# Kernel tuning notes

Measured on AMD Instinct MI355X. Metric: run time of the kernel, lower is better.

The kernel has to match this reference:

```python
import jax, jax.numpy as jnp
import numpy as np

SHOTS = 5  # kernel height of all convs; K must equal SHOTS


def _conv2d(x, w, b, stride, pad):
    # x: (N, C, H, W), w: (O, I, kh, kw)
    y = jax.lax.conv_general_dilated(
        x, w, window_strides=stride, padding=pad,
        dimension_numbers=("NCHW", "OIHW", "NCHW"))
    return y + b[None, :, None, None]


def setup_inputs() -> dict:
    key = jax.random.key(0)
    ks = jax.random.split(key, 10)
    B, N, K, D, NQ = 8, 20, SHOTS, 230, 200
    s = 0.05
    return {
        "S": jax.random.normal(ks[0], (B, N, K, D), jnp.float32),
        "Q": jax.random.normal(ks[1], (B, NQ, D), jnp.float32),
        "fc_w": jax.random.normal(ks[2], (D, D), jnp.float32) * s,
        "fc_b": jax.random.normal(ks[3], (D,), jnp.float32) * s,
        "conv1_w": jax.random.normal(ks[4], (32, 1, SHOTS, 1), jnp.float32) * s,
        "conv1_b": jax.random.normal(ks[5], (32,), jnp.float32) * s,
        "conv2_w": jax.random.normal(ks[6], (64, 32, SHOTS, 1), jnp.float32) * s,
        "conv2_b": jax.random.normal(ks[7], (64,), jnp.float32) * s,
        "convf_w": jax.random.normal(ks[8], (1, 64, SHOTS, 1), jnp.float32) * s,
        "convf_b": jax.random.normal(ks[9], (1,), jnp.float32) * s,
    }


def reference(S, Q, fc_w, fc_b, conv1_w, conv1_b, conv2_w, conv2_b, convf_w, convf_b):
    B, N, K, D = S.shape
    NQ = Q.shape[1]
    p = SHOTS // 2

    # ---- conv score extraction over the K (shot) axis ----
    x = S.reshape(B * N, 1, K, D)
    x = jax.nn.relu(_conv2d(x, conv1_w, conv1_b, (1, 1), [(p, p), (0, 0)]))
    x = jax.nn.relu(_conv2d(x, conv2_w, conv2_b, (1, 1), [(p, p), (0, 0)]))
    # dropout is identity in eval mode
    x = jax.nn.relu(_conv2d(x, convf_w, convf_b, (SHOTS, 1), [(0, 0), (0, 0)]))
    score = x.reshape(B, N, D)  # BxNxD

    # ---- hybrid attention prototype ----
    # fc applied to broadcast-expanded tensors == fc applied once, then broadcast
    Sf = S @ fc_w.T + fc_b            # B x N x K x D
    Qf = Q @ fc_w.T + fc_b            # B x NQ x D
    if K == 1:
        S_repre = jnp.broadcast_to(S.mean(-2)[:, None], (B, NQ, N, D))
    else:
        # tanh(S_fc * Q_fc).sum(-1) -> softmax over K
        t = jnp.tanh(Sf[:, None, :, :, :] * Qf[:, :, None, None, :])  # B,NQ,N,K,D
        att = jax.nn.softmax(t.sum(-1), axis=-1)                      # B,NQ,N,K
        S_repre = jnp.einsum("bqnk,bnkd->bqnd", att, S)               # B,NQ,N,D

    # ---- weighted squared L2 distance ----
    diff = S_repre - Q[:, :, None, :]                                  # B,NQ,N,D
    logits = -jnp.sum(diff * diff * score[:, None, :, :] * 700.0, axis=-1)  # B,NQ,N
    return (logits, S)
```

## Files before the change

### kernel.cpp

```cpp
#include <hip/hip_runtime.h>
#include <hip/hip_bf16.h>

typedef _Float16 f16x8 __attribute__((ext_vector_type(8)));
typedef float f32x4 __attribute__((ext_vector_type(4)));

#define BB 8
#define NN 20
#define KK 5
#define DD 230
#define NQ 200

#define NB_BFC 240
#define NB_BP  200
#define NB_CONV 575
#define NB_FC2 38
#define NB_ATT 800
#define NB_CP 90

__global__ void k_pre(const float* __restrict__ fc_w,
                      const float* __restrict__ w2, const float* __restrict__ b2,
                      const float* __restrict__ wf,
                      _Float16* __restrict__ Bfc, _Float16* __restrict__ Bp,
                      float2* __restrict__ tblg) {
    const int bid = blockIdx.x, tid = threadIdx.x;
    if (bid < NB_BFC) {
        int g = bid * 256 + tid;
        int kg = g & 31;
        int ncl = (g >> 5) & 15;
        int tk = g >> 9;
        int nt = tk >> 3, ks = tk & 7;
        int n = nt * 16 + ncl, k = ks * 32 + kg;
        float val = (n < DD && k < DD) ? fc_w[n * DD + k] : 0.f;
        Bfc[g] = (_Float16)val;
    } else {
        int g = (bid - NB_BFC) * 256 + tid;
        int kg = g & 31;
        int ncl = (g >> 5) & 15;
        int tk = g >> 9;
        int nt = tk / 5, ks = tk - nt * 5;
        int n = nt * 16 + ncl, k = ks * 32 + kg;
        int o = n / 5, i = n % 5;
        int c = k / 5, j = k - c * 5;
        int t = j - i + 2;
        float val = (t >= 0 && t < 5) ? w2[(o * 32 + c) * 5 + t] : 0.f;
        Bp[g] = (_Float16)val;
        if (g < 320) {
            int o2 = g / 5, i2 = g % 5;
            tblg[g] = make_float2(b2[o2], wf[o2 * 5 + i2]);
        }
    }
}

__global__ __launch_bounds__(512)
void k_main(const float* __restrict__ S, const float* __restrict__ Q,
            const float* __restrict__ w1, const float* __restrict__ b1,
            const _Float16* __restrict__ Bp, const _Float16* __restrict__ Bfc,
            const float2* __restrict__ tblg, float* __restrict__ sc,
            const float* __restrict__ fc_b,
            float* __restrict__ Sf, float* __restrict__ Qf) {
    __shared__ __align__(16) _Float16 XU[64 * 264];
    __shared__ float xfp[8][16];
    const int bid = blockIdx.x, tid = threadIdx.x;
    const int lane = tid & 63;
    const int w = __builtin_amdgcn_readfirstlane(tid >> 6);
    const int ncl = lane & 15;
    const int kg8 = (lane >> 4) * 8;
    const int g4 = lane >> 4;

    if (bid >= NB_CONV) {
        const int m0 = (bid - NB_CONV) * 64;
        for (int e = tid; e < 64 * 58; e += 512) {
            int row = e / 58, c4 = e - row * 58;
            int grow = m0 + row;
            float4 v = make_float4(0.f, 0.f, 0.f, 0.f);
            if (grow < 2400) {
                const float* inp = (grow < 800) ? S + (size_t)grow * DD
                                                : Q + (size_t)(grow - 800) * DD;
                if (c4 < 57) v = *(const float4*)&inp[c4 * 4];
                else { v.x = inp[228]; v.y = inp[229]; }
            }
            _Float16* xp = &XU[row * 264 + c4 * 4];
            xp[0] = (_Float16)v.x; xp[1] = (_Float16)v.y;
            xp[2] = (_Float16)v.z; xp[3] = (_Float16)v.w;
        }
        for (int e = tid; e < 64 * 16; e += 512) {
            int row = e >> 4, cc = 232 + (e & 15) * 2;
            *(unsigned int*)&XU[row * 264 + cc] = 0u;
        }
        __syncthreads();

        const int msub = w & 3;
        const int ngrp = w >> 2;
        f16x8 af[8];
#pragma unroll
        for (int ks = 0; ks < 8; ks++)
            af[ks] = *(const f16x8*)&XU[(msub * 16 + ncl) * 264 + ks * 32 + kg8];

        const int nt0 = ngrp * 8;
        const int ntn = ngrp ? 7 : 8;
        for (int ti = 0; ti < ntn; ti++) {
            const int nt = nt0 + ti;
            const _Float16* bp = Bfc + ((size_t)nt * 8 * 16) * 32;
            f32x4 a = {0.f, 0.f, 0.f, 0.f};
#pragma unroll
            for (int ks = 0; ks < 8; ks++) {
                f16x8 br = *(const f16x8*)&bp[(ks * 16 + ncl) * 32 + kg8];
                a = __builtin_amdgcn_mfma_f32_16x16x32_f16(af[ks], br, a, 0, 0, 0);
            }
            const int n = nt * 16 + ncl;
            const float bias = fc_b[n < DD ? n : DD - 1];
            if (n < DD) {
#pragma unroll
                for (int r = 0; r < 4; r++) {
                    int grow = m0 + msub * 16 + g4 * 4 + r;
                    if (grow < 800)
                        Sf[(size_t)grow * DD + n] = (a[r] + bias) * 2.8853900817779268f;
                    else if (grow < 2400)
                        Qf[(size_t)(grow - 800) * DD + n] = a[r] + bias;
                }
            }
        }
        return;
    }

    const int m0 = bid * 64;
    {
        const int m = m0 + lane;
        const int img = m / DD;
        const int d = m - img * DD;
        const float* sp = S + (size_t)img * KK * DD + d;
        float in5[5];
#pragma unroll
        for (int j = 0; j < 5; j++) in5[j] = sp[j * DD];
#pragma unroll
        for (int cc = 0; cc < 4; cc++) {
            int c = w * 4 + cc;
            float wl[5];
#pragma unroll
            for (int t = 0; t < 5; t++) wl[t] = w1[c * 5 + t];
            float bb = b1[c];
#pragma unroll
            for (int i = 0; i < 5; i++) {
                float a = bb;
#pragma unroll
                for (int t = 0; t < 5; t++) {
                    int j = i + t - 2;
                    if (j >= 0 && j < 5) a = fmaf(wl[t], in5[j], a);
                }
                XU[lane * 168 + c * 5 + i] = (_Float16)fmaxf(a, 0.f);
            }
        }
    }
    __syncthreads();

    const int msub = w & 3;
    const int gq = w >> 2;
    f16x8 af[5];
#pragma unroll
    for (int ks = 0; ks < 5; ks++)
        af[ks] = *(const f16x8*)&XU[(msub * 16 + ncl) * 168 + ks * 32 + kg8];

    float xf = 0.f;
    for (int t10 = 0; t10 < 10; t10++) {
        const int nt = gq * 10 + t10;
        const _Float16* bp = Bp + ((size_t)nt * 5 * 16) * 32;
        f32x4 a = {0.f, 0.f, 0.f, 0.f};
#pragma unroll
        for (int ks = 0; ks < 5; ks++) {
            f16x8 br = *(const f16x8*)&bp[(ks * 16 + ncl) * 32 + kg8];
            a = __builtin_amdgcn_mfma_f32_16x16x32_f16(br, af[ks], a, 0, 0, 0);
        }
        float2 tb[4];
#pragma unroll
        for (int r = 0; r < 4; r++) tb[r] = tblg[nt * 16 + g4 * 4 + r];
#pragma unroll
        for (int r = 0; r < 4; r++)
            xf = fmaf(fmaxf(a[r] + tb[r].x, 0.f), tb[r].y, xf);
    }
    xf += __shfl_xor(xf, 16, 64);
    xf += __shfl_xor(xf, 32, 64);
    if (lane < 16) xfp[w][lane] = xf;
    __syncthreads();
    if (tid < 64) {
        const int ms = tid >> 4, j = tid & 15;
        sc[m0 + ms * 16 + j] = xfp[ms][j] + xfp[ms + 4][j];
    }
}

__global__ __launch_bounds__(512)
void k_att(const float* __restrict__ Sf, const float* __restrict__ Qf,
           const float* __restrict__ S, const float* __restrict__ Q,
           const float* __restrict__ sc, const float* __restrict__ convf_b,
           float* __restrict__ out, float* __restrict__ Scopy) {
    __shared__ float Sft[25][232];
    __shared__ float Ls[8][25];
    const int bid = blockIdx.x, tid = threadIdx.x;
    if (bid >= NB_ATT) {
        int g = (bid - NB_ATT) * 512 + tid;
        if (g < 46000) ((float4*)Scopy)[g] = ((const float4*)S)[g];
        return;
    }
    const int lane = tid & 63, wv = tid >> 6;
    const int qg = bid % 25;
    const int nq = (bid / 25) & 3;
    const int b  = bid / 100;
    const int q  = qg * 8 + wv, n0 = nq * 5;
    const float LOG2E = 1.4426950408889634f;
    const float bf0 = convf_b[0];

    const float* sfb = Sf + ((size_t)b * 100 + n0 * 5) * DD;
    for (int e = tid; e < 25 * DD; e += 512) Sft[e / DD][e % DD] = sfb[e];
    __syncthreads();

    float qf[4];
    const float* qfp = Qf + ((size_t)b * NQ + q) * DD;
#pragma unroll
    for (int i = 0; i < 4; i++) {
        int d = lane + 64 * i;
        qf[i] = (d < DD) ? qfp[d] : 0.f;
    }
    for (int idx = 0; idx < 25; idx++) {
        float racc = 0.f;
#pragma unroll
        for (int i = 0; i < 4; i++) {
            int d = lane + 64 * i;
            float s = (d < DD) ? Sft[idx][d] : 0.f;
            float e = __builtin_amdgcn_exp2f(s * qf[i]);
            racc += __builtin_amdgcn_rcpf(e + 1.f);
        }
#pragma unroll
        for (int off = 32; off > 0; off >>= 1) racc += __shfl_xor(racc, off, 64);
        if (lane == 0) Ls[wv][idx] = fmaf(-2.f, racc, 256.f);
    }

    float qr[4];
    const float* qp = Q + ((size_t)b * NQ + q) * DD;
#pragma unroll
    for (int i = 0; i < 4; i++) {
        int d = lane + 64 * i;
        qr[i] = (d < DD) ? qp[d] : 0.f;
    }
    for (int nl = 0; nl < 5; nl++) {
        const float* lp = Ls[wv] + nl * 5;
        float v0 = lp[0], v1 = lp[1], v2 = lp[2], v3 = lp[3], v4 = lp[4];
        float m = fmaxf(fmaxf(fmaxf(v0, v1), fmaxf(v2, v3)), v4);
        float e0 = __builtin_amdgcn_exp2f((v0 - m) * LOG2E);
        float e1 = __builtin_amdgcn_exp2f((v1 - m) * LOG2E);
        float e2 = __builtin_amdgcn_exp2f((v2 - m) * LOG2E);
        float e3 = __builtin_amdgcn_exp2f((v3 - m) * LOG2E);
        float e4 = __builtin_amdgcn_exp2f((v4 - m) * LOG2E);
        float inv = __builtin_amdgcn_rcpf(e0 + e1 + e2 + e3 + e4);
        float a0 = e0 * inv, a1 = e1 * inv, a2 = e2 * inv, a3 = e3 * inv, a4 = e4 * inv;
        const int n = n0 + nl;
        const float* spn = S + (size_t)(b * NN + n) * KK * DD;
        const float* s0 = sc + (size_t)(b * NN + n) * DD;
        float acc = 0.f;
#pragma unroll
        for (int i = 0; i < 4; i++) {
            int d = lane + 64 * i;
            if (d < DD) {
                float rep = a0 * spn[d] + a1 * spn[DD + d] + a2 * spn[2 * DD + d]
                          + a3 * spn[3 * DD + d] + a4 * spn[4 * DD + d];
                float df = rep - qr[i];
                float scw = fmaxf(s0[d] + bf0, 0.f) * 700.f;
                acc = fmaf(df * df, scw, acc);
            }
        }
#pragma unroll
        for (int off = 32; off > 0; off >>= 1) acc += __shfl_xor(acc, off, 64);
        if (lane == 0) out[((size_t)b * NQ + q) * NN + n] = -acc;
    }
}

extern "C" void kernel_launch(void* const* d_in, const int* in_sizes, int n_in,
                              void* d_out, int out_size, void* d_ws, size_t ws_size,
                              hipStream_t stream) {
    const float* S       = (const float*)d_in[0];
    const float* Q       = (const float*)d_in[1];
    const float* fc_w    = (const float*)d_in[2];
    const float* fc_b    = (const float*)d_in[3];
    const float* conv1_w = (const float*)d_in[4];
    const float* conv1_b = (const float*)d_in[5];
    const float* conv2_w = (const float*)d_in[6];
    const float* conv2_b = (const float*)d_in[7];
    const float* convf_w = (const float*)d_in[8];
    const float* convf_b = (const float*)d_in[9];
    float* out = (float*)d_out;

    float* ws = (float*)d_ws;
    float* Sf  = ws;
    float* Qf  = Sf + 184000;
    float* sc  = Qf + 368000;
    _Float16* Bp  = (_Float16*)(sc + 36800);
    _Float16* Bfc = Bp + 51200;
    float2* tblg  = (float2*)(Bfc + 61440);

    k_pre<<<NB_BFC + NB_BP, 256, 0, stream>>>(
        fc_w, conv2_w, conv2_b, convf_w, Bfc, Bp, tblg);
    k_main<<<NB_CONV + NB_FC2, 512, 0, stream>>>(
        S, Q, conv1_w, conv1_b, Bp, Bfc, tblg, sc, fc_b, Sf, Qf);
    k_att<<<NB_ATT + NB_CP, 512, 0, stream>>>(
        Sf, Qf, S, Q, sc, convf_b, out, out + (size_t)BB * NQ * NN);
}
```

Measured before the change: 75.77 us.

## Restructure attention kernel to use MFMA row-sums over fp16 tanh tiles

The attention kernel now processes all 20 classes per block (200 blocks instead of 800). It stages all 100 Sf rows of a batch in shared memory as fp16, computes tanh values per element, and sums them with an MFMA against a ones vector instead of doing cross-lane shuffle reductions. Qf gets a padded row stride so it can be read with vector loads, and one loop in the conv kernel gets an unroll-2 pragma. The trade-offs are fp16 rounding of the tanh inputs and outputs, and fewer, larger blocks, which may lower occupancy.

```diff
diff --git a/kernel.cpp b/kernel.cpp
--- a/kernel.cpp
+++ b/kernel.cpp
@@ -9,13 +9,19 @@
 #define KK 5
 #define DD 230
 #define NQ 200
+#define QST 232
 
 #define NB_BFC 240
 #define NB_BP  200
 #define NB_CONV 575
 #define NB_FC2 38
-#define NB_ATT 800
+#define NB_ATT 200
 #define NB_CP 90
+
+static __device__ __forceinline__ unsigned int pk2(float a, float b) {
+    union { __fp16 h[2] __attribute__((aligned(4))); unsigned int u; } v;
+    v.h[0] = (__fp16)a; v.h[1] = (__fp16)b; return v.u;
+}
 
 __global__ void k_pre(const float* __restrict__ fc_w,
                       const float* __restrict__ w2, const float* __restrict__ b2,
@@ -116,7 +122,7 @@
                     if (grow < 800)
                         Sf[(size_t)grow * DD + n] = (a[r] + bias) * 2.8853900817779268f;
                     else if (grow < 2400)
-                        Qf[(size_t)(grow - 800) * DD + n] = a[r] + bias;
+                        Qf[(size_t)(grow - 800) * QST + n] = a[r] + bias;
                 }
             }
         }
@@ -161,6 +167,7 @@
         af[ks] = *(const f16x8*)&XU[(msub * 16 + ncl) * 168 + ks * 32 + kg8];
 
     float xf = 0.f;
+#pragma unroll 2
     for (int t10 = 0; t10 < 10; t10++) {
         const int nt = gq * 10 + t10;
         const _Float16* bp = Bp + ((size_t)nt * 5 * 16) * 32;
@@ -192,56 +199,79 @@
            const float* __restrict__ S, const float* __restrict__ Q,
            const float* __restrict__ sc, const float* __restrict__ convf_b,
            float* __restrict__ out, float* __restrict__ Scopy) {
-    __shared__ float Sft[25][232];
-    __shared__ float Ls[8][25];
+    __shared__ __align__(16) _Float16 SfT[112 * 264];
+    __shared__ __align__(16) float Lw[8][112];
     const int bid = blockIdx.x, tid = threadIdx.x;
     if (bid >= NB_ATT) {
         int g = (bid - NB_ATT) * 512 + tid;
         if (g < 46000) ((float4*)Scopy)[g] = ((const float4*)S)[g];
         return;
     }
-    const int lane = tid & 63, wv = tid >> 6;
-    const int qg = bid % 25;
-    const int nq = (bid / 25) & 3;
-    const int b  = bid / 100;
-    const int q  = qg * 8 + wv, n0 = nq * 5;
+    const int lane = tid & 63;
+    const int w = __builtin_amdgcn_readfirstlane(tid >> 6);
+    const int b = bid / 25, qg = bid % 25;
+    const int q = qg * 8 + w;
+    const int ncl = lane & 15;
+    const int g4 = lane >> 4;
+    const int kg8 = g4 * 8;
     const float LOG2E = 1.4426950408889634f;
     const float bf0 = convf_b[0];
 
-    const float* sfb = Sf + ((size_t)b * 100 + n0 * 5) * DD;
-    for (int e = tid; e < 25 * DD; e += 512) Sft[e / DD][e % DD] = sfb[e];
+    const float* sfb = Sf + (size_t)b * 100 * DD;
+    for (int e = tid; e < 112 * 132; e += 512) {
+        int row = e / 132, c2 = e - row * 132;
+        unsigned int u = 0u;
+        if (row < 100 && c2 <= 114) {
+            float2 v = *(const float2*)&sfb[row * DD + 2 * c2];
+            u = pk2(v.x, v.y);
+        }
+        *(unsigned int*)&SfT[row * 264 + 2 * c2] = u;
+    }
     __syncthreads();
 
-    float qf[4];
-    const float* qfp = Qf + ((size_t)b * NQ + q) * DD;
-#pragma unroll
-    for (int i = 0; i < 4; i++) {
-        int d = lane + 64 * i;
-        qf[i] = (d < DD) ? qfp[d] : 0.f;
-    }
-    for (int idx = 0; idx < 25; idx++) {
-        float racc = 0.f;
-#pragma unroll
-        for (int i = 0; i < 4; i++) {
-            int d = lane + 64 * i;
-            float s = (d < DD) ? Sft[idx][d] : 0.f;
-            float e = __builtin_amdgcn_exp2f(s * qf[i]);
-            racc += __builtin_amdgcn_rcpf(e + 1.f);
-        }
-#pragma unroll
-        for (int off = 32; off > 0; off >>= 1) racc += __shfl_xor(racc, off, 64);
-        if (lane == 0) Ls[wv][idx] = fmaf(-2.f, racc, 256.f);
+    f16x8 ones;
+#pragma unroll
+    for (int j = 0; j < 8; j++) ones[j] = (_Float16)1.f;
+    f32x4 acc[7];
+#pragma unroll
+    for (int t = 0; t < 7; t++) acc[t] = (f32x4){0.f, 0.f, 0.f, 0.f};
+
+    const float* qfp = Qf + (size_t)(b * NQ + q) * QST;
+    for (int ks = 0; ks < 8; ks++) {
+        f32x4 qa = *(const f32x4*)&qfp[ks * 32 + kg8];
+        f32x4 qb = *(const f32x4*)&qfp[ks * 32 + kg8 + 4];
+        float qv[8];
+#pragma unroll
+        for (int j = 0; j < 4; j++) { qv[j] = qa[j]; qv[4 + j] = qb[j]; }
+#pragma unroll
+        for (int t = 0; t < 7; t++) {
+            f16x8 s8 = *(const f16x8*)&SfT[(t * 16 + ncl) * 264 + ks * 32 + kg8];
+            f16x8 vf;
+#pragma unroll
+            for (int j = 0; j < 8; j++) {
+                float x = (float)s8[j] * qv[j];
+                float e = __builtin_amdgcn_exp2f(x);
+                float v = 1.f - 2.f * __builtin_amdgcn_rcpf(e + 1.f);
+                vf[j] = (_Float16)v;
+            }
+            acc[t] = __builtin_amdgcn_mfma_f32_16x16x32_f16(vf, ones, acc[t], 0, 0, 0);
+        }
+    }
+    if (ncl == 0) {
+#pragma unroll
+        for (int t = 0; t < 7; t++)
+            *(f32x4*)&Lw[w][t * 16 + g4 * 4] = acc[t];
     }
 
     float qr[4];
-    const float* qp = Q + ((size_t)b * NQ + q) * DD;
+    const float* qp = Q + (size_t)(b * NQ + q) * DD;
 #pragma unroll
     for (int i = 0; i < 4; i++) {
         int d = lane + 64 * i;
         qr[i] = (d < DD) ? qp[d] : 0.f;
     }
-    for (int nl = 0; nl < 5; nl++) {
-        const float* lp = Ls[wv] + nl * 5;
+    for (int n = 0; n < NN; n++) {
+        const float* lp = &Lw[w][n * 5];
         float v0 = lp[0], v1 = lp[1], v2 = lp[2], v3 = lp[3], v4 = lp[4];
         float m = fmaxf(fmaxf(fmaxf(v0, v1), fmaxf(v2, v3)), v4);
         float e0 = __builtin_amdgcn_exp2f((v0 - m) * LOG2E);
@@ -251,10 +281,9 @@
         float e4 = __builtin_amdgcn_exp2f((v4 - m) * LOG2E);
         float inv = __builtin_amdgcn_rcpf(e0 + e1 + e2 + e3 + e4);
         float a0 = e0 * inv, a1 = e1 * inv, a2 = e2 * inv, a3 = e3 * inv, a4 = e4 * inv;
-        const int n = n0 + nl;
         const float* spn = S + (size_t)(b * NN + n) * KK * DD;
         const float* s0 = sc + (size_t)(b * NN + n) * DD;
-        float acc = 0.f;
+        float acc2 = 0.f;
 #pragma unroll
         for (int i = 0; i < 4; i++) {
             int d = lane + 64 * i;
@@ -263,12 +292,12 @@
                           + a3 * spn[3 * DD + d] + a4 * spn[4 * DD + d];
                 float df = rep - qr[i];
                 float scw = fmaxf(s0[d] + bf0, 0.f) * 700.f;
-                acc = fmaf(df * df, scw, acc);
-            }
-        }
-#pragma unroll
-        for (int off = 32; off > 0; off >>= 1) acc += __shfl_xor(acc, off, 64);
-        if (lane == 0) out[((size_t)b * NQ + q) * NN + n] = -acc;
+                acc2 = fmaf(df * df, scw, acc2);
+            }
+        }
+#pragma unroll
+        for (int off = 32; off > 0; off >>= 1) acc2 += __shfl_xor(acc2, off, 64);
+        if (lane == 0) out[((size_t)b * NQ + q) * NN + n] = -acc2;
     }
 }
 
@@ -290,7 +319,7 @@
     float* ws = (float*)d_ws;
     float* Sf  = ws;
     float* Qf  = Sf + 184000;
-    float* sc  = Qf + 368000;
+    float* sc  = Qf + 371200;
     _Float16* Bp  = (_Float16*)(sc + 36800);
     _Float16* Bfc = Bp + 51200;
     float2* tblg  = (float2*)(Bfc + 61440);
```

Result: slower. 80.98 us (+6.9%).
